# Kernel tuning notes

Measured on AMD Instinct MI355X. Metric: run time of the kernel, lower is better.

The kernel has to match this reference:

```python
import jax, jax.numpy as jnp
import numpy as np

NV, NC, E, D = 100000, 400000, 1600000, 128

def _mlp2(x, w1, b1, w2, b2):
    # Linear->ReLU->Linear->ReLU (weights stored [in, out])
    return jax.nn.relu(jax.nn.relu(x @ w1 + b1) @ w2 + b2)

def setup_inputs() -> dict:
    key = jax.random.key(0)
    ks = jax.random.split(key, 16)
    s = 1.0 / np.sqrt(D)
    return {
        "hv": jax.random.normal(ks[0], (NV, D), jnp.float32),
        "hc": jax.random.normal(ks[1], (NC, D), jnp.float32),
        "row_v": jax.random.randint(ks[2], (E,), 0, NV, jnp.int32),
        "col_v": jax.random.randint(ks[3], (E,), 0, 2 * NC, jnp.int32),
        "row_c": jax.random.randint(ks[4], (E,), 0, NC, jnp.int32),
        "col_c": jax.random.randint(ks[5], (E,), 0, 2 * NV, jnp.int32),
        # message MLPs: order [fmv_pos, fmv_neg, fmc_pos, fmc_neg]
        "mw1": jax.random.normal(ks[6], (4, D, D), jnp.float32) * s,
        "mb1": jax.random.normal(ks[7], (4, D), jnp.float32) * s,
        "mw2": jax.random.normal(ks[8], (4, D, D), jnp.float32) * s,
        "mb2": jax.random.normal(ks[9], (4, D), jnp.float32) * s,
        # update MLPs: order [fuv, fuc]; first layer takes concat(h, m) -> 2D in
        "uw1": jax.random.normal(ks[10], (2, 2 * D, D), jnp.float32) * s,
        "ub1": jax.random.normal(ks[11], (2, D), jnp.float32) * s,
        "uw2": jax.random.normal(ks[12], (2, D, D), jnp.float32) * s,
        "ub2": jax.random.normal(ks[13], (2, D), jnp.float32) * s,
    }

def reference(hv, hc, row_v, col_v, row_c, col_c,
              mw1, mb1, mw2, mb2, uw1, ub1, uw2, ub2):
    nv, nc = hv.shape[0], hc.shape[0]
    # message: transform clause feats with pos/neg MLPs, concat rows, spmm via gather+segment_sum
    zv = jnp.concatenate([
        _mlp2(hc, mw1[0], mb1[0], mw2[0], mb2[0]),  # fmv_pos(hc)
        _mlp2(hc, mw1[1], mb1[1], mw2[1], mb2[1]),  # fmv_neg(hc)
    ], axis=0)                                       # [2*NC, D]
    mv = jax.ops.segment_sum(zv[col_v], row_v, num_segments=nv)  # spmm(vadj, zv)
    zc = jnp.concatenate([
        _mlp2(hv, mw1[2], mb1[2], mw2[2], mb2[2]),  # fmc_pos(hv)
        _mlp2(hv, mw1[3], mb1[3], mw2[3], mb2[3]),  # fmc_neg(hv)
    ], axis=0)                                       # [2*NV, D]
    mc = jax.ops.segment_sum(zc[col_c], row_c, num_segments=nc)  # spmm(cadj, zc)
    # update: concat(h, m) -> MLP
    hv_new = _mlp2(jnp.concatenate([hv, mv], axis=1), uw1[0], ub1[0], uw2[0], ub2[0])
    hc_new = _mlp2(jnp.concatenate([hc, mc], axis=1), uw1[1], ub1[1], uw2[1], ub2[1])
    return (hv_new, hc_new)
```

## Files before the change

kernel.cpp:

```cpp
#include <hip/hip_runtime.h>
#include <hip/hip_bf16.h>

#define NVV 100000
#define NCC 400000
#define NEE 1600000

typedef short short8 __attribute__((ext_vector_type(8)));
typedef short short4v __attribute__((ext_vector_type(4)));
typedef float f32x4 __attribute__((ext_vector_type(4)));
typedef unsigned int u32x2 __attribute__((ext_vector_type(2)));
typedef unsigned int u32x4 __attribute__((ext_vector_type(4)));

__device__ __forceinline__ float b2f(short s) {
    unsigned int u = ((unsigned int)(unsigned short)s) << 16;
    return __builtin_bit_cast(float, u);
}
__device__ __forceinline__ short f2b(float f) {
    __hip_bfloat16 h = __float2bfloat16(f);
    return __builtin_bit_cast(short, h);
}
__device__ __forceinline__ unsigned int cvtpk(float a, float b) {
    unsigned int r;
    asm("v_cvt_pk_bf16_f32 %0, %1, %2" : "=v"(r) : "v"(a), "v"(b));
    return r;
}
__device__ __forceinline__ short8 gload16(const short* p) {
    short8 d;
    asm volatile("global_load_dwordx4 %0, %1, off" : "=v"(d) : "v"(p));
    return d;
}
#define SB0() __builtin_amdgcn_sched_barrier(0)

__global__ __launch_bounds__(256)
void prep_all(const float* __restrict__ mw1, const float* __restrict__ mw2,
              const float* __restrict__ uw1, const float* __restrict__ uw2,
              short* __restrict__ wt_m1, short* __restrict__ wt_m2,
              short* __restrict__ wt_u1, short* __restrict__ wt_u2)
{
    int e = blockIdx.x * 256 + threadIdx.x;
    const float* W; short* WT; int K; int idx;
    if (e < 65536)        { W = mw1; WT = wt_m1; K = 128; idx = e; }
    else if (e < 131072)  { W = mw2; WT = wt_m2; K = 128; idx = e - 65536; }
    else if (e < 196608)  { W = uw1; WT = wt_u1; K = 256; idx = e - 131072; }
    else if (e < 229376)  { W = uw2; WT = wt_u2; K = 128; idx = e - 196608; }
    else return;
    int mk = idx >> 7, n = idx & 127;
    int mi = mk / K, k = mk - mi * K;
    WT[(size_t)mi * K * 128 + (size_t)n * K + k] = f2b(W[idx]);
}

__global__ __launch_bounds__(256)
void to_bf16_2(const float* __restrict__ hv, const float* __restrict__ hc,
               short* __restrict__ hvb, short* __restrict__ hcb)
{
    const long nv = (long)NVV * 128;
    const long nc = (long)NCC * 128;
    long i0 = ((long)blockIdx.x * 256 + threadIdx.x) * 8;
    long stride = (long)gridDim.x * 256 * 8;
    for (long i = i0; i < nv + nc; i += stride) {
        const float* in; short* outp; long j;
        if (i < nv) { in = hv; outp = hvb; j = i; }
        else        { in = hc; outp = hcb; j = i - nv; }
        f32x4 a = *(const f32x4*)(in + j);
        f32x4 b = *(const f32x4*)(in + j + 4);
        u32x4 o;
        o[0] = cvtpk(a[0], a[1]);
        o[1] = cvtpk(a[2], a[3]);
        o[2] = cvtpk(b[0], b[1]);
        o[3] = cvtpk(b[2], b[3]);
        *(u32x4*)(outp + j) = o;
    }
}

template<int NW>
__global__ __launch_bounds__(NW * 64, 1)
void mlp2_msg_all(const short* __restrict__ hcb, const short* __restrict__ hvb,
                  const short* __restrict__ WT1, const float* __restrict__ B1a,
                  const short* __restrict__ WT2, const float* __restrict__ B2a,
                  short* __restrict__ zv, short* __restrict__ zc, int splitC)
{
    constexpr int BM = NW * 32;
    constexpr int NT = NW * 64;
    __shared__ short sW1[128 * 136];
    __shared__ short sW2[128 * 136];
    __shared__ short sH[BM * 136];

    const int tid = threadIdx.x;
    const int lane = tid & 63;
    const int w = tid >> 6;
    const int p = lane & 15;
    const int q = lane >> 4;

    int b = blockIdx.x;
    const short* X; short* z; int M, c0, cstr, set;
    if (b < splitC) {
        set = b & 1; X = hcb; z = zv + (size_t)set * NCC * 128;
        M = NCC; c0 = b >> 1; cstr = splitC >> 1;
    } else {
        int bb = b - splitC;
        set = 2 + (bb & 1); X = hvb; z = zc + (size_t)(bb & 1) * NVV * 128;
        M = NVV; c0 = bb >> 1; cstr = (gridDim.x - splitC) >> 1;
    }
    const int nChunks = (M + BM - 1) / BM;

    const short* w1g = WT1 + set * 16384;
    const short* w2g = WT2 + set * 16384;
    const float* b1g = B1a + set * 128;
    const float* b2g = B2a + set * 128;

    for (int e = tid * 8; e < 128 * 128; e += NT * 8) {
        int n = e >> 7, k = e & 127;
        *(short8*)(sW1 + n * 136 + k) = *(const short8*)(w1g + e);
        *(short8*)(sW2 + n * 136 + k) = *(const short8*)(w2g + e);
    }
    __syncthreads();

    if (c0 >= nChunks) return;

    short8 xfA[2][4], xfB[2][4];

    auto issueX = [&](short8 (&xf)[2][4], int c) {
        long base = (long)c * BM + w * 32;
        #pragma unroll
        for (int t = 0; t < 2; ++t) {
            long m = base + t * 16 + p;
            if (m > (long)M - 1) m = (long)M - 1;
            const short* src = X + m * 128 + q * 8;
            #pragma unroll
            for (int kk = 0; kk < 4; ++kk)
                xf[t][kk] = gload16(src + kk * 32);
        }
        SB0();
    };

    auto computeStore = [&](const short8 (&xf)[2][4], int c) {
        long base = (long)c * BM + w * 32;
        f32x4 acc[8][2];
        #pragma unroll
        for (int cc = 0; cc < 8; ++cc)
            #pragma unroll
            for (int t = 0; t < 2; ++t)
                acc[cc][t] = (f32x4){0.f, 0.f, 0.f, 0.f};

        #pragma unroll
        for (int kk = 0; kk < 4; ++kk) {
            short8 af[8];
            #pragma unroll
            for (int cc = 0; cc < 8; ++cc)
                af[cc] = *(const short8*)(sW1 + (cc * 16 + p) * 136 + kk * 32 + q * 8);
            #pragma unroll
            for (int cc = 0; cc < 8; ++cc)
                #pragma unroll
                for (int t = 0; t < 2; ++t)
                    acc[cc][t] = __builtin_amdgcn_mfma_f32_16x16x32_bf16(af[cc], xf[t][kk], acc[cc][t], 0, 0, 0);
        }

        #pragma unroll
        for (int cc = 0; cc < 8; ++cc) {
            f32x4 bb = *(const f32x4*)(b1g + cc * 16 + q * 4);
            #pragma unroll
            for (int t = 0; t < 2; ++t) {
                u32x2 u;
                u[0] = cvtpk(fmaxf(acc[cc][t][0] + bb[0], 0.f), fmaxf(acc[cc][t][1] + bb[1], 0.f));
                u[1] = cvtpk(fmaxf(acc[cc][t][2] + bb[2], 0.f), fmaxf(acc[cc][t][3] + bb[3], 0.f));
                *(u32x2*)(sH + (w * 32 + t * 16 + p) * 136 + cc * 16 + q * 4) = u;
            }
        }
        asm volatile("s_waitcnt lgkmcnt(0)" ::: "memory");

        f32x4 acc2[8][2];
        #pragma unroll
        for (int cc = 0; cc < 8; ++cc)
            #pragma unroll
            for (int t = 0; t < 2; ++t)
                acc2[cc][t] = (f32x4){0.f, 0.f, 0.f, 0.f};

        #pragma unroll
        for (int kk = 0; kk < 4; ++kk) {
            short8 af[8], bfr[2];
            #pragma unroll
            for (int cc = 0; cc < 8; ++cc)
                af[cc] = *(const short8*)(sW2 + (cc * 16 + p) * 136 + kk * 32 + q * 8);
            #pragma unroll
            for (int t = 0; t < 2; ++t)
                bfr[t] = *(const short8*)(sH + (w * 32 + t * 16 + p) * 136 + kk * 32 + q * 8);
            #pragma unroll
            for (int cc = 0; cc < 8; ++cc)
                #pragma unroll
                for (int t = 0; t < 2; ++t)
                    acc2[cc][t] = __builtin_amdgcn_mfma_f32_16x16x32_bf16(af[cc], bfr[t], acc2[cc][t], 0, 0, 0);
        }

        #pragma unroll
        for (int cc = 0; cc < 8; ++cc) {
            f32x4 bb = *(const f32x4*)(b2g + cc * 16 + q * 4);
            #pragma unroll
            for (int t = 0; t < 2; ++t) {
                long m = base + t * 16 + p;
                if (m < M) {
                    u32x2 u;
                    u[0] = cvtpk(fmaxf(acc2[cc][t][0] + bb[0], 0.f), fmaxf(acc2[cc][t][1] + bb[1], 0.f));
                    u[1] = cvtpk(fmaxf(acc2[cc][t][2] + bb[2], 0.f), fmaxf(acc2[cc][t][3] + bb[3], 0.f));
                    *(u32x2*)(z + m * 128 + cc * 16 + q * 4) = u;
                }
            }
        }
    };

    int c = c0;
    issueX(xfA, c);
    asm volatile("s_waitcnt vmcnt(0)" ::: "memory");
    SB0();
    while (true) {
        {
            bool hn = (c + cstr < nChunks);
            if (hn) issueX(xfB, c + cstr);
            computeStore(xfA, c);
            c += cstr;
            if (!hn) return;
            asm volatile("s_waitcnt vmcnt(16)" ::: "memory");
            SB0();
        }
        {
            bool hn = (c + cstr < nChunks);
            if (hn) issueX(xfA, c + cstr);
            computeStore(xfB, c);
            c += cstr;
            if (!hn) return;
            asm volatile("s_waitcnt vmcnt(16)" ::: "memory");
            SB0();
        }
    }
}

template<int NW>
__global__ __launch_bounds__(NW * 64, 1)
void mlp2_upd_all(const short* __restrict__ hvb, const short* __restrict__ hcb,
                  const short* __restrict__ mv, const short* __restrict__ mc,
                  const short* __restrict__ wt_u1, const float* __restrict__ ub1,
                  const short* __restrict__ wt_u2, const float* __restrict__ ub2,
                  float* __restrict__ out, int splitV)
{
    constexpr int BM = NW * 32;
    constexpr int NT = NW * 64;
    __shared__ short sW1[128 * 264];
    __shared__ short sW2[128 * 136];
    __shared__ short sH[BM * 136];

    const int tid = threadIdx.x;
    const int lane = tid & 63;
    const int w = tid >> 6;
    const int p = lane & 15;
    const int q = lane >> 4;

    int b = blockIdx.x;
    const short *X, *X2; float* O; int M, c0, cstr, set;
    if (b < splitV) {
        set = 0; X = hvb; X2 = mv; O = out; M = NVV; c0 = b; cstr = splitV;
    } else {
        set = 1; X = hcb; X2 = mc; O = out + (size_t)NVV * 128; M = NCC;
        c0 = b - splitV; cstr = gridDim.x - splitV;
    }
    const int nChunks = (M + BM - 1) / BM;

    const short* W1T = wt_u1 + set * 32768;
    const short* W2T = wt_u2 + set * 16384;
    const float* B1 = ub1 + set * 128;
    const float* B2 = ub2 + set * 128;

    for (int e = tid * 8; e < 128 * 256; e += NT * 8) {
        int n = e >> 8, k = e & 255;
        *(short8*)(sW1 + n * 264 + k) = *(const short8*)(W1T + e);
    }
    for (int e = tid * 8; e < 128 * 128; e += NT * 8) {
        int n = e >> 7, k = e & 127;
        *(short8*)(sW2 + n * 136 + k) = *(const short8*)(W2T + e);
    }
    __syncthreads();

    if (c0 >= nChunks) return;

    short8 hA[2][4], hB[2][4], mr[2][4];

    auto issueH = [&](short8 (&h)[2][4], int c) {
        long base = (long)c * BM + w * 32;
        #pragma unroll
        for (int t = 0; t < 2; ++t) {
            long m = base + t * 16 + p;
            if (m > (long)M - 1) m = (long)M - 1;
            const short* s1 = X + m * 128 + q * 8;
            #pragma unroll
            for (int kk = 0; kk < 4; ++kk)
                h[t][kk] = gload16(s1 + kk * 32);
        }
        SB0();
    };
    auto issueM = [&](int c) {
        long base = (long)c * BM + w * 32;
        #pragma unroll
        for (int t = 0; t < 2; ++t) {
            long m = base + t * 16 + p;
            if (m > (long)M - 1) m = (long)M - 1;
            const short* s2 = X2 + m * 128 + q * 8;
            #pragma unroll
            for (int kk = 0; kk < 4; ++kk)
                mr[t][kk] = gload16(s2 + kk * 32);
        }
        SB0();
    };

    auto body = [&](const short8 (&h)[2][4], int c, bool hn, int cn) {
        long base = (long)c * BM + w * 32;
        f32x4 acc[8][2];
        #pragma unroll
        for (int cc = 0; cc < 8; ++cc)
            #pragma unroll
            for (int t = 0; t < 2; ++t)
                acc[cc][t] = (f32x4){0.f, 0.f, 0.f, 0.f};

        #pragma unroll
        for (int kk = 0; kk < 8; ++kk) {
            short8 af[8];
            #pragma unroll
            for (int cc = 0; cc < 8; ++cc)
                af[cc] = *(const short8*)(sW1 + (cc * 16 + p) * 264 + kk * 32 + q * 8);
            #pragma unroll
            for (int cc = 0; cc < 8; ++cc)
                #pragma unroll
                for (int t = 0; t < 2; ++t) {
                    short8 xcur = (kk < 4) ? h[t][kk] : mr[t][kk - 4];
                    acc[cc][t] = __builtin_amdgcn_mfma_f32_16x16x32_bf16(af[cc], xcur, acc[cc][t], 0, 0, 0);
                }
        }

        if (hn) issueM(cn);

        #pragma unroll
        for (int cc = 0; cc < 8; ++cc) {
            f32x4 bb = *(const f32x4*)(B1 + cc * 16 + q * 4);
            #pragma unroll
            for (int t = 0; t < 2; ++t) {
                u32x2 u;
                u[0] = cvtpk(fmaxf(acc[cc][t][0] + bb[0], 0.f), fmaxf(acc[cc][t][1] + bb[1], 0.f));
                u[1] = cvtpk(fmaxf(acc[cc][t][2] + bb[2], 0.f), fmaxf(acc[cc][t][3] + bb[3], 0.f));
                *(u32x2*)(sH + (w * 32 + t * 16 + p) * 136 + cc * 16 + q * 4) = u;
            }
        }
        asm volatile("s_waitcnt lgkmcnt(0)" ::: "memory");

        f32x4 acc2[8][2];
        #pragma unroll
        for (int cc = 0; cc < 8; ++cc)
            #pragma unroll
            for (int t = 0; t < 2; ++t)
                acc2[cc][t] = (f32x4){0.f, 0.f, 0.f, 0.f};

        #pragma unroll
        for (int kk = 0; kk < 4; ++kk) {
            short8 af[8], bfr[2];
            #pragma unroll
            for (int cc = 0; cc < 8; ++cc)
                af[cc] = *(const short8*)(sW2 + (cc * 16 + p) * 136 + kk * 32 + q * 8);
            #pragma unroll
            for (int t = 0; t < 2; ++t)
                bfr[t] = *(const short8*)(sH + (w * 32 + t * 16 + p) * 136 + kk * 32 + q * 8);
            #pragma unroll
            for (int cc = 0; cc < 8; ++cc)
                #pragma unroll
                for (int t = 0; t < 2; ++t)
                    acc2[cc][t] = __builtin_amdgcn_mfma_f32_16x16x32_bf16(af[cc], bfr[t], acc2[cc][t], 0, 0, 0);
        }

        #pragma unroll
        for (int cc = 0; cc < 8; ++cc) {
            f32x4 bb = *(const f32x4*)(B2 + cc * 16 + q * 4);
            #pragma unroll
            for (int t = 0; t < 2; ++t) {
                long m = base + t * 16 + p;
                if (m < M) {
                    f32x4 fv;
                    #pragma unroll
                    for (int i = 0; i < 4; ++i)
                        fv[i] = fmaxf(acc2[cc][t][i] + bb[i], 0.f);
                    *(f32x4*)(O + m * 128 + cc * 16 + q * 4) = fv;
                }
            }
        }
    };

    int c = c0;
    issueH(hA, c);
    issueM(c);
    asm volatile("s_waitcnt vmcnt(0)" ::: "memory");
    SB0();
    while (true) {
        {
            bool hn = (c + cstr < nChunks);
            if (hn) issueH(hB, c + cstr);
            body(hA, c, hn, c + cstr);
            c += cstr;
            if (!hn) return;
            asm volatile("s_waitcnt vmcnt(16)" ::: "memory");
            SB0();
        }
        {
            bool hn = (c + cstr < nChunks);
            if (hn) issueH(hA, c + cstr);
            body(hB, c, hn, c + cstr);
            c += cstr;
            if (!hn) return;
            asm volatile("s_waitcnt vmcnt(16)" ::: "memory");
            SB0();
        }
    }
}

__global__ __launch_bounds__(256)
void hist_xcd(const int* __restrict__ row_v, const int* __restrict__ row_c,
              int* __restrict__ cnt_v, int* __restrict__ cnt_c)
{
    const int g = blockIdx.x & 7;
    const int bg = blockIdx.x >> 3, nbg = gridDim.x >> 3;
    const int r0 = g * (NVV / 8), r1 = r0 + NVV / 8;
    for (int e = bg * 256 + threadIdx.x; e < NEE; e += nbg * 256) {
        int r = row_v[e];
        if (r >= r0 && r < r1) atomicAdd(&cnt_v[r], 1);
    }
    const int s0 = g * (NCC / 8), s1 = s0 + NCC / 8;
    for (int e = bg * 256 + threadIdx.x; e < NEE; e += nbg * 256) {
        int r = row_c[e];
        if (r >= s0 && r < s1) atomicAdd(&cnt_c[r], 1);
    }
}

__global__ __launch_bounds__(256)
void seg_reduce2(const int* __restrict__ cnt_v, const int* __restrict__ cnt_c,
                 int* __restrict__ bsum_v, int* __restrict__ bsum_c, int Bv)
{
    __shared__ int s[256];
    int b = blockIdx.x, t = threadIdx.x;
    const int* counts; int* bsum; int N; int bb;
    if (b < Bv) { counts = cnt_v; bsum = bsum_v; N = NVV; bb = b; }
    else        { counts = cnt_c; bsum = bsum_c; N = NCC; bb = b - Bv; }
    int base = bb * 512;
    int v = 0;
    if (base + t < N) v += counts[base + t];
    if (base + 256 + t < N) v += counts[base + 256 + t];
    s[t] = v;
    __syncthreads();
    for (int off = 128; off > 0; off >>= 1) {
        if (t < off) s[t] += s[t + off];
        __syncthreads();
    }
    if (t == 0) bsum[bb] = s[0];
}

__global__ __launch_bounds__(1024)
void scan_bsum2(int* __restrict__ bsum_v, int* __restrict__ bsum_c, int Bv, int Bc)
{
    __shared__ int s[1024];
    int* bsum = (blockIdx.x == 0) ? bsum_v : bsum_c;
    int B = (blockIdx.x == 0) ? Bv : Bc;
    int t = threadIdx.x;
    s[t] = (t < B) ? bsum[t] : 0;
    __syncthreads();
    for (int off = 1; off < 1024; off <<= 1) {
        int v = (t >= off) ? s[t - off] : 0;
        __syncthreads();
        s[t] += v;
        __syncthreads();
    }
    if (t < B) bsum[t] = (t == 0) ? 0 : s[t - 1];
}

__global__ __launch_bounds__(512)
void scan_final2(const int* __restrict__ cnt_v, const int* __restrict__ cnt_c,
                 const int* __restrict__ bsum_v, const int* __restrict__ bsum_c,
                 int* __restrict__ offs_v, int* __restrict__ offs_c, int Bv)
{
    __shared__ int s[512];
    int b = blockIdx.x, t = threadIdx.x;
    const int* counts; const int* bsum; int* offs; int N; int bb;
    if (b < Bv) { counts = cnt_v; bsum = bsum_v; offs = offs_v; N = NVV; bb = b; }
    else        { counts = cnt_c; bsum = bsum_c; offs = offs_c; N = NCC; bb = b - Bv; }
    int idx = bb * 512 + t;
    int c = (idx < N) ? counts[idx] : 0;
    s[t] = c;
    __syncthreads();
    for (int off = 1; off < 512; off <<= 1) {
        int v = (t >= off) ? s[t - off] : 0;
        __syncthreads();
        s[t] += v;
        __syncthreads();
    }
    if (idx < N) offs[idx] = bsum[bb] + s[t] - c;
    if (idx == N - 1) offs[N] = bsum[bb] + s[t];
}

__global__ __launch_bounds__(256)
void csr_fill_xcd(const int* __restrict__ row_v, const int* __restrict__ col_v,
                  const int* __restrict__ row_c, const int* __restrict__ col_c,
                  const int* __restrict__ offs_v, const int* __restrict__ offs_c,
                  int* __restrict__ cur_v, int* __restrict__ cur_c,
                  int* __restrict__ edge_v, int* __restrict__ edge_c)
{
    const int g = blockIdx.x & 7;
    const int bg = blockIdx.x >> 3, nbg = gridDim.x >> 3;
    const int r0 = g * (NVV / 8), r1 = r0 + NVV / 8;
    for (int e = bg * 256 + threadIdx.x; e < NEE; e += nbg * 256) {
        int r = row_v[e];
        if (r >= r0 && r < r1) {
            int pos = offs_v[r] + atomicAdd(&cur_v[r], 1);
            edge_v[pos] = col_v[e];
        }
    }
    const int s0 = g * (NCC / 8), s1 = s0 + NCC / 8;
    for (int e = bg * 256 + threadIdx.x; e < NEE; e += nbg * 256) {
        int r = row_c[e];
        if (r >= s0 && r < s1) {
            int pos = offs_c[r] + atomicAdd(&cur_c[r], 1);
            edge_c[pos] = col_c[e];
        }
    }
}

__global__ __launch_bounds__(256)
void csr_gather_all(const short* __restrict__ zv, const short* __restrict__ zc,
                    const int* __restrict__ offs_v, const int* __restrict__ edge_v,
                    const int* __restrict__ offs_c, const int* __restrict__ edge_c,
                    short* __restrict__ mv, short* __restrict__ mc)
{
    int wid = (int)((blockIdx.x * 256 + threadIdx.x) >> 6);
    int lane = threadIdx.x & 63;
    int sub = lane >> 4;
    int sl = lane & 15;
    int row = wid * 4 + sub;
    if (row >= NVV + NCC) return;

    const short* z; const int* offs; const int* ec; short* md; int r;
    if (row < NVV) { z = zv; offs = offs_v; ec = edge_v; md = mv; r = row; }
    else           { z = zc; offs = offs_c; ec = edge_c; md = mc; r = row - NVV; }

    int beg = offs[r], end = offs[r + 1];

    float a[8];
    #pragma unroll
    for (int i = 0; i < 8; ++i) a[i] = 0.f;

    int j = beg;
    for (; j + 3 < end; j += 4) {
        int c0 = ec[j], c1 = ec[j + 1], c2 = ec[j + 2], c3 = ec[j + 3];
        short8 v0 = *(const short8*)(z + (long)c0 * 128 + sl * 8);
        short8 v1 = *(const short8*)(z + (long)c1 * 128 + sl * 8);
        short8 v2 = *(const short8*)(z + (long)c2 * 128 + sl * 8);
        short8 v3 = *(const short8*)(z + (long)c3 * 128 + sl * 8);
        #pragma unroll
        for (int i = 0; i < 8; ++i)
            a[i] += (b2f(v0[i]) + b2f(v1[i])) + (b2f(v2[i]) + b2f(v3[i]));
    }
    for (; j < end; ++j) {
        int c = ec[j];
        short8 v = *(const short8*)(z + (long)c * 128 + sl * 8);
        #pragma unroll
        for (int i = 0; i < 8; ++i) a[i] += b2f(v[i]);
    }

    u32x4 o;
    o[0] = cvtpk(a[0], a[1]);
    o[1] = cvtpk(a[2], a[3]);
    o[2] = cvtpk(a[4], a[5]);
    o[3] = cvtpk(a[6], a[7]);
    *(u32x4*)(md + (long)r * 128 + sl * 8) = o;
}

extern "C" void kernel_launch(void* const* d_in, const int* in_sizes, int n_in,
                              void* d_out, int out_size, void* d_ws, size_t ws_size,
                              hipStream_t stream)
{
    const float* hv   = (const float*)d_in[0];
    const float* hc   = (const float*)d_in[1];
    const int* row_v  = (const int*)d_in[2];
    const int* col_v  = (const int*)d_in[3];
    const int* row_c  = (const int*)d_in[4];
    const int* col_c  = (const int*)d_in[5];
    const float* mw1  = (const float*)d_in[6];
    const float* mb1  = (const float*)d_in[7];
    const float* mw2  = (const float*)d_in[8];
    const float* mb2  = (const float*)d_in[9];
    const float* uw1  = (const float*)d_in[10];
    const float* ub1  = (const float*)d_in[11];
    const float* uw2  = (const float*)d_in[12];
    const float* ub2  = (const float*)d_in[13];
    float* out = (float*)d_out;

    short* zv = (short*)d_ws;
    short* zc = zv + (size_t)2 * NCC * 128;
    short* mv = zc + (size_t)2 * NVV * 128;
    short* mc = mv + (size_t)NVV * 128;
    short* wt_m1 = mc + (size_t)NCC * 128;
    short* wt_m2 = wt_m1 + 4 * 16384;
    short* wt_u1 = wt_m2 + 4 * 16384;
    short* wt_u2 = wt_u1 + 2 * 32768;
    short* hvb = wt_u2 + 2 * 16384;
    short* hcb = hvb + (size_t)NVV * 128;
    int* edge_v = (int*)(hcb + (size_t)NCC * 128);
    int* edge_c = edge_v + NEE;
    int* offs_v = edge_c + NEE;
    int* offs_c = offs_v + (NVV + 1);
    int* cnt_v  = offs_c + (NCC + 1);
    int* cnt_c  = cnt_v + NVV;
    int* bsum_v = cnt_c + NCC;
    int* bsum_c = bsum_v + 1024;

    const int Bv = (NVV + 511) / 512;
    const int Bc = (NCC + 511) / 512;

    prep_all<<<(229376 + 255) / 256, 256, 0, stream>>>(
        mw1, mw2, uw1, uw2, wt_m1, wt_m2, wt_u1, wt_u2);
    to_bf16_2<<<2048, 256, 0, stream>>>(hv, hc, hvb, hcb);

    hipMemsetAsync(cnt_v, 0, (NVV + NCC) * sizeof(int), stream);
    hist_xcd<<<1024, 256, 0, stream>>>(row_v, row_c, cnt_v, cnt_c);
    seg_reduce2<<<Bv + Bc, 256, 0, stream>>>(cnt_v, cnt_c, bsum_v, bsum_c, Bv);
    scan_bsum2<<<2, 1024, 0, stream>>>(bsum_v, bsum_c, Bv, Bc);
    scan_final2<<<Bv + Bc, 512, 0, stream>>>(cnt_v, cnt_c, bsum_v, bsum_c, offs_v, offs_c, Bv);
    hipMemsetAsync(cnt_v, 0, (NVV + NCC) * sizeof(int), stream);
    csr_fill_xcd<<<1024, 256, 0, stream>>>(
        row_v, col_v, row_c, col_c, offs_v, offs_c, cnt_v, cnt_c, edge_v, edge_c);

    mlp2_msg_all<8><<<256, 512, 0, stream>>>(
        hcb, hvb, wt_m1, mb1, wt_m2, mb2, zv, zc, 204);

    csr_gather_all<<<((NVV + NCC) / 4 + 3) / 4, 256, 0, stream>>>(
        zv, zc, offs_v, edge_v, offs_c, edge_c, mv, mc);

    mlp2_upd_all<6><<<256, 384, 0, stream>>>(
        hvb, hcb, mv, mc, wt_u1, ub1, wt_u2, ub2, out, 51);
}
```

Baseline: 1.144 ms.

## Fuse prep kernels into one launch, shrink LDS padding, widen update kernel

Merges the histogram, the bf16 input conversion and the weight transpose into a single phase1 launch. It also replaces the second memset with a separate cursor buffer that is zeroed by one up-front memset. The update MLP's LDS row strides shrink from 264/136 to 260/132, which frees shared memory so the kernel can run with 7 waves instead of 6. This cuts launch overhead and lets independent prep work overlap. The new LDS strides may change bank-conflict behaviour, and the shorter padding could raise conflicts on the 16-byte reads.

```diff
diff --git a/kernel.cpp b/kernel.cpp
--- a/kernel.cpp
+++ b/kernel.cpp
@@ -32,43 +32,58 @@
 #define SB0() __builtin_amdgcn_sched_barrier(0)
 
 __global__ __launch_bounds__(256)
-void prep_all(const float* __restrict__ mw1, const float* __restrict__ mw2,
-              const float* __restrict__ uw1, const float* __restrict__ uw2,
-              short* __restrict__ wt_m1, short* __restrict__ wt_m2,
-              short* __restrict__ wt_u1, short* __restrict__ wt_u2)
-{
-    int e = blockIdx.x * 256 + threadIdx.x;
-    const float* W; short* WT; int K; int idx;
-    if (e < 65536)        { W = mw1; WT = wt_m1; K = 128; idx = e; }
-    else if (e < 131072)  { W = mw2; WT = wt_m2; K = 128; idx = e - 65536; }
-    else if (e < 196608)  { W = uw1; WT = wt_u1; K = 256; idx = e - 131072; }
-    else if (e < 229376)  { W = uw2; WT = wt_u2; K = 128; idx = e - 196608; }
-    else return;
-    int mk = idx >> 7, n = idx & 127;
-    int mi = mk / K, k = mk - mi * K;
-    WT[(size_t)mi * K * 128 + (size_t)n * K + k] = f2b(W[idx]);
-}
-
-__global__ __launch_bounds__(256)
-void to_bf16_2(const float* __restrict__ hv, const float* __restrict__ hc,
-               short* __restrict__ hvb, short* __restrict__ hcb)
-{
-    const long nv = (long)NVV * 128;
-    const long nc = (long)NCC * 128;
-    long i0 = ((long)blockIdx.x * 256 + threadIdx.x) * 8;
-    long stride = (long)gridDim.x * 256 * 8;
-    for (long i = i0; i < nv + nc; i += stride) {
-        const float* in; short* outp; long j;
-        if (i < nv) { in = hv; outp = hvb; j = i; }
-        else        { in = hc; outp = hcb; j = i - nv; }
-        f32x4 a = *(const f32x4*)(in + j);
-        f32x4 b = *(const f32x4*)(in + j + 4);
-        u32x4 o;
-        o[0] = cvtpk(a[0], a[1]);
-        o[1] = cvtpk(a[2], a[3]);
-        o[2] = cvtpk(b[0], b[1]);
-        o[3] = cvtpk(b[2], b[3]);
-        *(u32x4*)(outp + j) = o;
+void phase1(const int* __restrict__ row_v, const int* __restrict__ row_c,
+            int* __restrict__ cnt_v, int* __restrict__ cnt_c,
+            const float* __restrict__ hv, const float* __restrict__ hc,
+            short* __restrict__ hvb, short* __restrict__ hcb,
+            const float* __restrict__ mw1, const float* __restrict__ mw2,
+            const float* __restrict__ uw1, const float* __restrict__ uw2,
+            short* __restrict__ wt_m1, short* __restrict__ wt_m2,
+            short* __restrict__ wt_u1, short* __restrict__ wt_u2)
+{
+    int b = blockIdx.x;
+    if (b < 1024) {
+        const int g = b & 7;
+        const int bg = b >> 3, nbg = 128;
+        const int r0 = g * (NVV / 8), r1 = r0 + NVV / 8;
+        for (int e = bg * 256 + threadIdx.x; e < NEE; e += nbg * 256) {
+            int r = row_v[e];
+            if (r >= r0 && r < r1) atomicAdd(&cnt_v[r], 1);
+        }
+        const int s0 = g * (NCC / 8), s1 = s0 + NCC / 8;
+        for (int e = bg * 256 + threadIdx.x; e < NEE; e += nbg * 256) {
+            int r = row_c[e];
+            if (r >= s0 && r < s1) atomicAdd(&cnt_c[r], 1);
+        }
+    } else if (b < 3072) {
+        const long nv = (long)NVV * 128;
+        const long nc = (long)NCC * 128;
+        long i0 = ((long)(b - 1024) * 256 + threadIdx.x) * 8;
+        long stride = (long)2048 * 256 * 8;
+        for (long i = i0; i < nv + nc; i += stride) {
+            const float* in; short* outp; long j;
+            if (i < nv) { in = hv; outp = hvb; j = i; }
+            else        { in = hc; outp = hcb; j = i - nv; }
+            f32x4 a = *(const f32x4*)(in + j);
+            f32x4 bq = *(const f32x4*)(in + j + 4);
+            u32x4 o;
+            o[0] = cvtpk(a[0], a[1]);
+            o[1] = cvtpk(a[2], a[3]);
+            o[2] = cvtpk(bq[0], bq[1]);
+            o[3] = cvtpk(bq[2], bq[3]);
+            *(u32x4*)(outp + j) = o;
+        }
+    } else {
+        int e = (b - 3072) * 256 + threadIdx.x;
+        const float* W; short* WT; int K; int idx;
+        if (e < 65536)        { W = mw1; WT = wt_m1; K = 128; idx = e; }
+        else if (e < 131072)  { W = mw2; WT = wt_m2; K = 128; idx = e - 65536; }
+        else if (e < 196608)  { W = uw1; WT = wt_u1; K = 256; idx = e - 131072; }
+        else if (e < 229376)  { W = uw2; WT = wt_u2; K = 128; idx = e - 196608; }
+        else return;
+        int mk = idx >> 7, n = idx & 127;
+        int mi = mk / K, k = mk - mi * K;
+        WT[(size_t)mi * K * 128 + (size_t)n * K + k] = f2b(W[idx]);
     }
 }
 
@@ -243,9 +258,9 @@
 {
     constexpr int BM = NW * 32;
     constexpr int NT = NW * 64;
-    __shared__ short sW1[128 * 264];
-    __shared__ short sW2[128 * 136];
-    __shared__ short sH[BM * 136];
+    __shared__ short sW1[128 * 260];
+    __shared__ short sW2[128 * 132];
+    __shared__ short sH[BM * 132];
 
     const int tid = threadIdx.x;
     const int lane = tid & 63;
@@ -270,11 +285,11 @@
 
     for (int e = tid * 8; e < 128 * 256; e += NT * 8) {
         int n = e >> 8, k = e & 255;
-        *(short8*)(sW1 + n * 264 + k) = *(const short8*)(W1T + e);
+        *(short8*)(sW1 + n * 260 + k) = *(const short8*)(W1T + e);
     }
     for (int e = tid * 8; e < 128 * 128; e += NT * 8) {
         int n = e >> 7, k = e & 127;
-        *(short8*)(sW2 + n * 136 + k) = *(const short8*)(W2T + e);
+        *(short8*)(sW2 + n * 132 + k) = *(const short8*)(W2T + e);
     }
     __syncthreads();
 
@@ -323,7 +338,7 @@
             short8 af[8];
             #pragma unroll
             for (int cc = 0; cc < 8; ++cc)
-                af[cc] = *(const short8*)(sW1 + (cc * 16 + p) * 264 + kk * 32 + q * 8);
+                af[cc] = *(const short8*)(sW1 + (cc * 16 + p) * 260 + kk * 32 + q * 8);
             #pragma unroll
             for (int cc = 0; cc < 8; ++cc)
                 #pragma unroll
@@ -343,7 +358,7 @@
                 u32x2 u;
                 u[0] = cvtpk(fmaxf(acc[cc][t][0] + bb[0], 0.f), fmaxf(acc[cc][t][1] + bb[1], 0.f));
                 u[1] = cvtpk(fmaxf(acc[cc][t][2] + bb[2], 0.f), fmaxf(acc[cc][t][3] + bb[3], 0.f));
-                *(u32x2*)(sH + (w * 32 + t * 16 + p) * 136 + cc * 16 + q * 4) = u;
+                *(u32x2*)(sH + (w * 32 + t * 16 + p) * 132 + cc * 16 + q * 4) = u;
             }
         }
         asm volatile("s_waitcnt lgkmcnt(0)" ::: "memory");
@@ -360,10 +375,10 @@
             short8 af[8], bfr[2];
             #pragma unroll
             for (int cc = 0; cc < 8; ++cc)
-                af[cc] = *(const short8*)(sW2 + (cc * 16 + p) * 136 + kk * 32 + q * 8);
+                af[cc] = *(const short8*)(sW2 + (cc * 16 + p) * 132 + kk * 32 + q * 8);
             #pragma unroll
             for (int t = 0; t < 2; ++t)
-                bfr[t] = *(const short8*)(sH + (w * 32 + t * 16 + p) * 136 + kk * 32 + q * 8);
+                bfr[t] = *(const short8*)(sH + (w * 32 + t * 16 + p) * 132 + kk * 32 + q * 8);
             #pragma unroll
             for (int cc = 0; cc < 8; ++cc)
                 #pragma unroll
@@ -415,23 +430,6 @@
     }
 }
 
-__global__ __launch_bounds__(256)
-void hist_xcd(const int* __restrict__ row_v, const int* __restrict__ row_c,
-              int* __restrict__ cnt_v, int* __restrict__ cnt_c)
-{
-    const int g = blockIdx.x & 7;
-    const int bg = blockIdx.x >> 3, nbg = gridDim.x >> 3;
-    const int r0 = g * (NVV / 8), r1 = r0 + NVV / 8;
-    for (int e = bg * 256 + threadIdx.x; e < NEE; e += nbg * 256) {
-        int r = row_v[e];
-        if (r >= r0 && r < r1) atomicAdd(&cnt_v[r], 1);
-    }
-    const int s0 = g * (NCC / 8), s1 = s0 + NCC / 8;
-    for (int e = bg * 256 + threadIdx.x; e < NEE; e += nbg * 256) {
-        int r = row_c[e];
-        if (r >= s0 && r < s1) atomicAdd(&cnt_c[r], 1);
-    }
-}
 
 __global__ __launch_bounds__(256)
 void seg_reduce2(const int* __restrict__ cnt_v, const int* __restrict__ cnt_c,
@@ -609,24 +607,27 @@
     int* offs_c = offs_v + (NVV + 1);
     int* cnt_v  = offs_c + (NCC + 1);
     int* cnt_c  = cnt_v + NVV;
-    int* bsum_v = cnt_c + NCC;
+    int* cur_v  = cnt_c + NCC;
+    int* cur_c  = cur_v + NVV;
+    int* bsum_v = cur_c + NCC;
     int* bsum_c = bsum_v + 1024;
 
     const int Bv = (NVV + 511) / 512;
     const int Bc = (NCC + 511) / 512;
 
-    prep_all<<<(229376 + 255) / 256, 256, 0, stream>>>(
+    hipMemsetAsync(cnt_v, 0, 2 * (NVV + NCC) * sizeof(int), stream);
+
+    phase1<<<3968, 256, 0, stream>>>(
+        row_v, row_c, cnt_v, cnt_c,
+        hv, hc, hvb, hcb,
         mw1, mw2, uw1, uw2, wt_m1, wt_m2, wt_u1, wt_u2);
-    to_bf16_2<<<2048, 256, 0, stream>>>(hv, hc, hvb, hcb);
-
-    hipMemsetAsync(cnt_v, 0, (NVV + NCC) * sizeof(int), stream);
-    hist_xcd<<<1024, 256, 0, stream>>>(row_v, row_c, cnt_v, cnt_c);
+
     seg_reduce2<<<Bv + Bc, 256, 0, stream>>>(cnt_v, cnt_c, bsum_v, bsum_c, Bv);
     scan_bsum2<<<2, 1024, 0, stream>>>(bsum_v, bsum_c, Bv, Bc);
     scan_final2<<<Bv + Bc, 512, 0, stream>>>(cnt_v, cnt_c, bsum_v, bsum_c, offs_v, offs_c, Bv);
-    hipMemsetAsync(cnt_v, 0, (NVV + NCC) * sizeof(int), stream);
+
     csr_fill_xcd<<<1024, 256, 0, stream>>>(
-        row_v, col_v, row_c, col_c, offs_v, offs_c, cnt_v, cnt_c, edge_v, edge_c);
+        row_v, col_v, row_c, col_c, offs_v, offs_c, cur_v, cur_c, edge_v, edge_c);
 
     mlp2_msg_all<8><<<256, 512, 0, stream>>>(
         hcb, hvb, wt_m1, mb1, wt_m2, mb2, zv, zc, 204);
@@ -634,6 +635,6 @@
     csr_gather_all<<<((NVV + NCC) / 4 + 3) / 4, 256, 0, stream>>>(
         zv, zc, offs_v, edge_v, offs_c, edge_c, mv, mc);
 
-    mlp2_upd_all<6><<<256, 384, 0, stream>>>(
+    mlp2_upd_all<7><<<256, 448, 0, stream>>>(
         hvb, hcb, mv, mc, wt_u1, ub1, wt_u2, ub2, out, 51);
 }
```

Measured after the change: 1.061 ms, median of 2. 1.08x faster.
